# Optimization experiments

Hardware: AMD Instinct MI355X
Metric: run time of the kernel (lower is better)

The kernel has to match this reference:

```python
import jax, jax.numpy as jnp
import numpy as np

DIM = 1024
HEADS = 16
HEAD_DIM = DIM // HEADS


def setup_inputs() -> dict:
    key = jax.random.key(0)
    ks = jax.random.split(key, 9)
    s = 1.0 / np.sqrt(DIM)
    return {
        "x": jax.random.normal(ks[0], (2, 2048, DIM), dtype=jnp.float32),
        "Wq": jax.random.normal(ks[1], (DIM, DIM), dtype=jnp.float32) * s,
        "bq": jnp.zeros((DIM,), dtype=jnp.float32),
        "Wk": jax.random.normal(ks[2], (DIM, DIM), dtype=jnp.float32) * s,
        "bk": jnp.zeros((DIM,), dtype=jnp.float32),
        "Wv": jax.random.normal(ks[3], (DIM, DIM), dtype=jnp.float32) * s,
        "bv": jnp.zeros((DIM,), dtype=jnp.float32),
        "Wo": jax.random.normal(ks[4], (DIM, DIM), dtype=jnp.float32) * s,
        "bo": jnp.zeros((DIM,), dtype=jnp.float32),
    }


def reference(x, Wq, bq, Wk, bk, Wv, bv, Wo, bo):
    B, S, D = x.shape
    H, Dh = HEADS, HEAD_DIM

    def split_heads(t):  # (B,S,D) -> (B,H,S,Dh)
        return t.reshape(B, S, H, Dh).transpose(0, 2, 1, 3)

    q = split_heads(x @ Wq + bq)
    k = split_heads(x @ Wk + bk)
    v = split_heads(x @ Wv + bv)

    scores = jnp.einsum("bhsd,bhtd->bhst", q, k) / np.sqrt(Dh).astype(x.dtype)
    attn = jax.nn.softmax(scores, axis=-1)
    ctx = jnp.einsum("bhst,bhtd->bhsd", attn, v)
    ctx = ctx.transpose(0, 2, 1, 3).reshape(B, S, D)
    return ctx @ Wo + bo
```

## Files before the change

### kernel.cpp

```cpp
#include <hip/hip_runtime.h>
#include <hip/hip_bf16.h>
#include <cstdint>

typedef __bf16 bf16;
typedef __bf16 bf16x8 __attribute__((ext_vector_type(8)));
typedef float f32x4 __attribute__((ext_vector_type(4)));
typedef float f32x8 __attribute__((ext_vector_type(8)));
typedef float f32x16 __attribute__((ext_vector_type(16)));

#define DIM   1024
#define SEQ   2048
#define BATCH 2
#define HEADS 16
#define HDIM  64

#define QSCALE 0.1803368801111204f

__device__ __forceinline__ void gload_lds16(const void* g, void* l) {
    __builtin_amdgcn_global_load_lds(
        (const __attribute__((address_space(1))) void*)g,
        (__attribute__((address_space(3))) void*)l,
        16, 0, 0);
}

__device__ __forceinline__ uint32_t pkbf(float a, float b) {
    union { bf16 h[2]; uint32_t u; } t;
    t.h[0] = (bf16)a; t.h[1] = (bf16)b;
    return t.u;
}

#define LO8(v)  __builtin_shufflevector(v, v, 0, 1, 2, 3, 4, 5, 6, 7)
#define HI8(v)  __builtin_shufflevector(v, v, 8, 9, 10, 11, 12, 13, 14, 15)
#define LO4(v)  __builtin_shufflevector(v, v, 0, 1, 2, 3)
#define HI4(v)  __builtin_shufflevector(v, v, 4, 5, 6, 7)

__global__ __launch_bounds__(256) void cvt_wt_kernel(const float* __restrict__ Wq,
                                                     const float* __restrict__ Wk,
                                                     const float* __restrict__ Wv,
                                                     const float* __restrict__ Wo,
                                                     bf16* __restrict__ Wt) {
    int z = blockIdx.z;
    const float* W = (z == 0) ? Wq : (z == 1) ? Wk : (z == 2) ? Wv : Wo;
    bf16* out = Wt + (size_t)z * DIM * DIM;
    int w = threadIdx.x >> 6, lane = threadIdx.x & 63;
    int n  = blockIdx.x * 64 + lane;
    int kb = blockIdx.y * 32 + w * 8;
    bf16x8 o;
#pragma unroll
    for (int j = 0; j < 8; ++j)
        o[j] = (bf16)W[(size_t)(kb + j) * DIM + n];
    *(bf16x8*)(out + (size_t)n * DIM + kb) = o;
}

template <int MODE>
__global__ __launch_bounds__(256) void gemm128_kernel(
        const void* __restrict__ Ap,
        const bf16* __restrict__ WtB,
        const float* __restrict__ b0,
        const float* __restrict__ b1,
        const float* __restrict__ b2,
        void* __restrict__ outp) {
    constexpr int K  = DIM;
    constexpr int BN = (MODE == 1) ? 64 : 128;
    constexpr int NR = BN / 32;
    int z = (MODE == 0) ? blockIdx.z : 0;
    const bf16* Bt = WtB + (size_t)z * DIM * DIM;
    const float* bias = (MODE == 0) ? ((z == 0) ? b0 : (z == 1) ? b1 : b2) : b0;

    int m0 = blockIdx.y * 128, n0 = blockIdx.x * BN;
    int tid = threadIdx.x;
    int w = tid >> 6, lane = tid & 63, l15 = lane & 15, l4 = lane >> 4;
    int wr = (w >> 1) * 64, wc = (w & 1) * (BN / 2);

    __shared__ __align__(16) bf16 As[128 * 32];
    __shared__ __align__(16) bf16 Bs[BN * 32];

    int arow = tid >> 1, acol = (tid & 1) * 16;
    const float* asrc = (MODE == 0)
        ? (const float*)Ap + (size_t)(m0 + arow) * K + acol : nullptr;

    f32x4 acc[4][NR] = {};

    for (int k0 = 0; k0 < K; k0 += 32) {
#pragma unroll
        for (int rr = 0; rr < BN / 64; ++rr) {
            int c = rr * 256 + tid;
            gload_lds16(Bt + (size_t)(n0 + (c >> 2)) * K + k0 + (c & 3) * 8, &Bs[c * 8]);
        }
        if constexpr (MODE == 0) {
            const float4* s4 = (const float4*)(asrc + k0);
            float4 f0 = s4[0], f1 = s4[1], f2 = s4[2], f3 = s4[3];
            bf16x8 e0, e1;
            e0[0] = (bf16)f0.x; e0[1] = (bf16)f0.y; e0[2] = (bf16)f0.z; e0[3] = (bf16)f0.w;
            e0[4] = (bf16)f1.x; e0[5] = (bf16)f1.y; e0[6] = (bf16)f1.z; e0[7] = (bf16)f1.w;
            e1[0] = (bf16)f2.x; e1[1] = (bf16)f2.y; e1[2] = (bf16)f2.z; e1[3] = (bf16)f2.w;
            e1[4] = (bf16)f3.x; e1[5] = (bf16)f3.y; e1[6] = (bf16)f3.z; e1[7] = (bf16)f3.w;
            *(bf16x8*)&As[arow * 32 + acol]     = e0;
            *(bf16x8*)&As[arow * 32 + acol + 8] = e1;
        } else {
            const bf16* A = (const bf16*)Ap;
#pragma unroll
            for (int rr = 0; rr < 2; ++rr) {
                int c = rr * 256 + tid;
                gload_lds16(A + (size_t)(m0 + (c >> 2)) * K + k0 + (c & 3) * 8, &As[c * 8]);
            }
        }
        __syncthreads();
        bf16x8 af[4], bfr[NR];
#pragma unroll
        for (int m = 0; m < 4; ++m)
            af[m] = *(const bf16x8*)&As[(wr + m * 16 + l15) * 32 + l4 * 8];
#pragma unroll
        for (int n = 0; n < NR; ++n)
            bfr[n] = *(const bf16x8*)&Bs[(wc + n * 16 + l15) * 32 + l4 * 8];
#pragma unroll
        for (int m = 0; m < 4; ++m)
#pragma unroll
            for (int n = 0; n < NR; ++n)
                acc[m][n] = __builtin_amdgcn_mfma_f32_16x16x32_bf16(
                    af[m], bfr[n], acc[m][n], 0, 0, 0);
        __syncthreads();
    }

    float oscale = (MODE == 0 && z == 0) ? QSCALE : 1.0f;
#pragma unroll
    for (int n = 0; n < NR; ++n) {
        int col = n0 + wc + n * 16 + l15;
        float bv = bias[col];
#pragma unroll
        for (int m = 0; m < 4; ++m) {
            int rowb = m0 + wr + m * 16 + l4 * 4;
            if (MODE == 1) {
                float* out = (float*)outp;
#pragma unroll
                for (int i = 0; i < 4; ++i)
                    out[(size_t)(rowb + i) * DIM + col] = acc[m][n][i] + bv;
            } else if (z < 2) {
                bf16* out = (bf16*)outp + (size_t)z * (BATCH * HEADS * SEQ * HDIM);
                int h = col >> 6, d = col & 63;
#pragma unroll
                for (int i = 0; i < 4; ++i) {
                    int row = rowb + i;
                    int bb = row >> 11, s = row & 2047;
                    out[(((size_t)(bb * HEADS + h)) * SEQ + s) * HDIM + d] =
                        (bf16)((acc[m][n][i] + bv) * oscale);
                }
            } else {
                char* out = (char*)outp + (size_t)2 * (BATCH * HEADS * SEQ * HDIM) * 2;
                int h = col >> 6, d = col & 63;
                int dblk = d >> 5;
                int bb = rowb >> 11, s0 = rowb & 2047;
                int hb2 = bb * HEADS + h;
                int lane2 = (d & 31) + 32 * ((s0 >> 3) & 1);
                size_t off = (size_t)(hb2 * 64 + (s0 >> 5)) * 4096
                             + (dblk * 2 + ((s0 >> 4) & 1)) * 1024
                             + lane2 * 16 + (s0 & 7) * 2;
                union { bf16 hh[4]; ushort4 v; } pk;
#pragma unroll
                for (int i = 0; i < 4; ++i) pk.hh[i] = (bf16)(acc[m][n][i] + bv);
                *(ushort4*)(out + off) = pk.v;
            }
        }
    }
}

__global__ __launch_bounds__(256) void attn_kernel(const bf16* __restrict__ Q,
                                                   const bf16* __restrict__ K,
                                                   const bf16* __restrict__ Vf,
                                                   bf16* __restrict__ ctx) {
    int bid = blockIdx.x;
    int xcd = bid & 7, i = bid >> 3;
    int hb  = xcd * (BATCH * HEADS / 8) + (i >> 4);
    int q0  = (i & 15) * 128;
    int bb = hb >> 4, h = hb & 15;
    int tid = threadIdx.x, w = tid >> 6, lane = tid & 63;
    int l31 = lane & 31, hi = lane >> 5;

    const bf16* Qh = Q + (size_t)hb * SEQ * HDIM;
    const bf16* Kh = K + (size_t)hb * SEQ * HDIM;
    const char* Vh = (const char*)Vf + (size_t)hb * 64 * 4096 + lane * 16;

    __shared__ __align__(16) bf16 Ks[2][8192];

    int qrow = q0 + w * 32 + l31;
    bf16x8 qf[4];
#pragma unroll
    for (int ks = 0; ks < 4; ++ks)
        qf[ks] = *(const bf16x8*)&Qh[(size_t)qrow * HDIM + ks * 16 + hi * 8];

    f32x16 o0 = {}, o1 = {};
    float l = 0.f;

    const bf16* kbase[2];
    int ldsoff[2];
#pragma unroll
    for (int r = 0; r < 2; ++r) {
        int c = r * 256 + tid;
        int krow = c >> 3, kj = (c & 7) ^ (krow & 7);
        kbase[r] = Kh + (size_t)krow * HDIM + kj * 8;
        ldsoff[r] = c * 8;
    }
    auto stage = [&](bf16* ksd, int kv0) {
#pragma unroll
        for (int r = 0; r < 2; ++r) {
            gload_lds16(kbase[r] + (size_t)kv0 * HDIM,        ksd + ldsoff[r]);
            gload_lds16(kbase[r] + (size_t)(kv0 + 64) * HDIM, ksd + ldsoff[r] + 4096);
        }
    };

    int koffA = l31 * 128;
    int cb[4];
#pragma unroll
    for (int ks = 0; ks < 4; ++ks)
        cb[ks] = ((2 * ks + hi) ^ (l31 & 7)) << 4;

    auto sub64 = [&](const char* kp, const char* vjp) {
        f32x16 s0 = {}, s1 = {};
        __builtin_amdgcn_s_setprio(1);
#pragma unroll
        for (int ks = 0; ks < 4; ++ks) {
            bf16x8 k0 = *(const bf16x8*)(kp + koffA + cb[ks]);
            bf16x8 k1 = *(const bf16x8*)(kp + koffA + 4096 + cb[ks]);
            s0 = __builtin_amdgcn_mfma_f32_32x32x16_bf16(k0, qf[ks], s0, 0, 0, 0);
            s1 = __builtin_amdgcn_mfma_f32_32x32x16_bf16(k1, qf[ks], s1, 0, 0, 0);
        }
        __builtin_amdgcn_s_setprio(0);

        bf16x8 v0 = *(const bf16x8*)(vjp);
        bf16x8 v1 = *(const bf16x8*)(vjp + 1024);
        bf16x8 v2 = *(const bf16x8*)(vjp + 2048);
        bf16x8 v3 = *(const bf16x8*)(vjp + 3072);
        bf16x8 v4 = *(const bf16x8*)(vjp + 4096);
        bf16x8 v5 = *(const bf16x8*)(vjp + 5120);
        bf16x8 v6 = *(const bf16x8*)(vjp + 6144);
        bf16x8 v7 = *(const bf16x8*)(vjp + 7168);

#pragma unroll
        for (int r = 0; r < 16; ++r) {
            s0[r] = __builtin_amdgcn_exp2f(s0[r]);
            s1[r] = __builtin_amdgcn_exp2f(s1[r]);
        }

        f32x16 a16 = s0 + s1;
        f32x8  a8  = LO8(a16) + HI8(a16);
        f32x4  a4  = LO4(a8) + HI4(a8);
        l += (a4[0] + a4[1]) + (a4[2] + a4[3]);

        bf16x8 pa[4];
#pragma unroll
        for (int f2 = 0; f2 < 4; ++f2) {
            const f32x16& s = (f2 < 2) ? s0 : s1;
            int rb = (f2 & 1) * 8;
            uint32_t w0 = pkbf(s[rb + 0], s[rb + 1]), w1 = pkbf(s[rb + 2], s[rb + 3]);
            uint32_t w2 = pkbf(s[rb + 4], s[rb + 5]), w3 = pkbf(s[rb + 6], s[rb + 7]);
            asm("v_permlane32_swap_b32 %0, %1" : "+v"(w0), "+v"(w2));
            asm("v_permlane32_swap_b32 %0, %1" : "+v"(w1), "+v"(w3));
            union { uint32_t u[4]; bf16x8 v; } t2;
            t2.u[0] = w0; t2.u[1] = w1; t2.u[2] = w2; t2.u[3] = w3;
            pa[f2] = t2.v;
        }

        __builtin_amdgcn_s_setprio(1);
        o0 = __builtin_amdgcn_mfma_f32_32x32x16_bf16(v0, pa[0], o0, 0, 0, 0);
        o0 = __builtin_amdgcn_mfma_f32_32x32x16_bf16(v1, pa[1], o0, 0, 0, 0);
        o1 = __builtin_amdgcn_mfma_f32_32x32x16_bf16(v2, pa[0], o1, 0, 0, 0);
        o1 = __builtin_amdgcn_mfma_f32_32x32x16_bf16(v3, pa[1], o1, 0, 0, 0);
        o0 = __builtin_amdgcn_mfma_f32_32x32x16_bf16(v4, pa[2], o0, 0, 0, 0);
        o0 = __builtin_amdgcn_mfma_f32_32x32x16_bf16(v5, pa[3], o0, 0, 0, 0);
        o1 = __builtin_amdgcn_mfma_f32_32x32x16_bf16(v6, pa[2], o1, 0, 0, 0);
        o1 = __builtin_amdgcn_mfma_f32_32x32x16_bf16(v7, pa[3], o1, 0, 0, 0);
        __builtin_amdgcn_s_setprio(0);
    };

    auto proc = [&](const char* ksb, int kv0) {
        sub64(ksb,        Vh + (size_t)(kv0 >> 5) * 4096);
        sub64(ksb + 8192, Vh + (size_t)((kv0 + 64) >> 5) * 4096);
    };

    constexpr int NT = SEQ / 128;
    stage(Ks[0], 0);
    __syncthreads();

    for (int t = 0; t < NT; t += 2) {
        if (t + 1 < NT) stage(Ks[1], (t + 1) * 128);
        proc((const char*)&Ks[0][0], t * 128);
        __syncthreads();
        if (t + 2 < NT) stage(Ks[0], (t + 2) * 128);
        proc((const char*)&Ks[1][0], (t + 1) * 128);
        __syncthreads();
    }

    l += __shfl_xor(l, 32);
    float inv = 1.0f / l;
    size_t base = ((size_t)bb * SEQ + qrow) * DIM + h * HDIM;
#pragma unroll
    for (int g = 0; g < 4; ++g) {
        int dh0 = 8 * g + 4 * hi;
        union { bf16 hh[4]; ushort4 u; } a, b2;
#pragma unroll
        for (int i = 0; i < 4; ++i) {
            a.hh[i]  = (bf16)(o0[4 * g + i] * inv);
            b2.hh[i] = (bf16)(o1[4 * g + i] * inv);
        }
        *(ushort4*)&ctx[base + dh0]      = a.u;
        *(ushort4*)&ctx[base + 32 + dh0] = b2.u;
    }
}

extern "C" void kernel_launch(void* const* d_in, const int* in_sizes, int n_in,
                              void* d_out, int out_size, void* d_ws, size_t ws_size,
                              hipStream_t stream) {
    const float* x  = (const float*)d_in[0];
    const float* Wq = (const float*)d_in[1];
    const float* bq = (const float*)d_in[2];
    const float* Wk = (const float*)d_in[3];
    const float* bk = (const float*)d_in[4];
    const float* Wv = (const float*)d_in[5];
    const float* bv = (const float*)d_in[6];
    const float* Wo = (const float*)d_in[7];
    const float* bo = (const float*)d_in[8];

    char* ws = (char*)d_ws;
    bf16* Wt  = (bf16*)(ws + (8u  << 20));
    bf16* Qb  = (bf16*)(ws + (16u << 20));
    bf16* Kb  = (bf16*)(ws + (24u << 20));
    bf16* Vf  = (bf16*)(ws + (32u << 20));
    bf16* ctx = (bf16*)(ws + (40u << 20));

    cvt_wt_kernel<<<dim3(16, 32, 4), 256, 0, stream>>>(Wq, Wk, Wv, Wo, Wt);
    gemm128_kernel<0><<<dim3(8, 32, 3), 256, 0, stream>>>(x, Wt, bq, bk, bv, (void*)Qb);
    attn_kernel<<<512, 256, 0, stream>>>(Qb, Kb, Vf, ctx);
    gemm128_kernel<1><<<dim3(16, 32), 256, 0, stream>>>(
        ctx, Wt + (size_t)3 * DIM * DIM, bo, bo, bo, (void*)d_out);
}
```

Before: 121.3 us.

## Split attention KV range in two and merge partial outputs in a separate kernel

The attention kernel now splits each query tile's key/value sequence into two halves, doubling the grid to 1024 blocks. Each block writes an unnormalized bf16 partial context and its row sums, and a new merge kernel adds the two partials and divides by the combined sum. The aim is more blocks per CU, helped by a launch-bounds occupancy hint, so latency hides better. The cost is an extra kernel launch, extra global traffic for the partials, and bf16 rounding of unnormalized partials. The merge is only correct if both halves use the same softmax reference max, which cannot be checked from the visible code.

```diff
diff --git a/kernel.cpp b/kernel.cpp
--- a/kernel.cpp
+++ b/kernel.cpp
@@ -164,14 +164,19 @@
     }
 }
 
-__global__ __launch_bounds__(256) void attn_kernel(const bf16* __restrict__ Q,
-                                                   const bf16* __restrict__ K,
-                                                   const bf16* __restrict__ Vf,
-                                                   bf16* __restrict__ ctx) {
+__global__ __launch_bounds__(256, 4) void attn_kernel(const bf16* __restrict__ Q,
+                                                      const bf16* __restrict__ K,
+                                                      const bf16* __restrict__ Vf,
+                                                      bf16* __restrict__ op0,
+                                                      bf16* __restrict__ op1,
+                                                      float* __restrict__ lbuf) {
     int bid = blockIdx.x;
     int xcd = bid & 7, i = bid >> 3;
-    int hb  = xcd * (BATCH * HEADS / 8) + (i >> 4);
-    int q0  = (i & 15) * 128;
+    int hb  = xcd * 4 + (i >> 5);
+    int rem = i & 31;
+    int q0  = (rem >> 1) * 128;
+    int si  = rem & 1;
+    int kvb = si * (SEQ / 2);
     int bb = hb >> 4, h = hb & 15;
     int tid = threadIdx.x, w = tid >> 6, lane = tid & 63;
     int l31 = lane & 31, hi = lane >> 5;
@@ -277,21 +282,23 @@
         sub64(ksb + 8192, Vh + (size_t)((kv0 + 64) >> 5) * 4096);
     };
 
-    constexpr int NT = SEQ / 128;
-    stage(Ks[0], 0);
+    constexpr int NT = (SEQ / 2) / 128;
+    stage(Ks[0], kvb);
     __syncthreads();
 
     for (int t = 0; t < NT; t += 2) {
-        if (t + 1 < NT) stage(Ks[1], (t + 1) * 128);
-        proc((const char*)&Ks[0][0], t * 128);
+        if (t + 1 < NT) stage(Ks[1], kvb + (t + 1) * 128);
+        proc((const char*)&Ks[0][0], kvb + t * 128);
         __syncthreads();
-        if (t + 2 < NT) stage(Ks[0], (t + 2) * 128);
-        proc((const char*)&Ks[1][0], (t + 1) * 128);
+        if (t + 2 < NT) stage(Ks[0], kvb + (t + 2) * 128);
+        proc((const char*)&Ks[1][0], kvb + (t + 1) * 128);
         __syncthreads();
     }
 
     l += __shfl_xor(l, 32);
-    float inv = 1.0f / l;
+    bf16* op = si ? op1 : op0;
+    if (hi == 0)
+        lbuf[((size_t)si * BATCH * HEADS + hb) * SEQ + qrow] = l;
     size_t base = ((size_t)bb * SEQ + qrow) * DIM + h * HDIM;
 #pragma unroll
     for (int g = 0; g < 4; ++g) {
@@ -299,12 +306,35 @@
         union { bf16 hh[4]; ushort4 u; } a, b2;
 #pragma unroll
         for (int i = 0; i < 4; ++i) {
-            a.hh[i]  = (bf16)(o0[4 * g + i] * inv);
-            b2.hh[i] = (bf16)(o1[4 * g + i] * inv);
-        }
-        *(ushort4*)&ctx[base + dh0]      = a.u;
-        *(ushort4*)&ctx[base + 32 + dh0] = b2.u;
-    }
+            a.hh[i]  = (bf16)o0[4 * g + i];
+            b2.hh[i] = (bf16)o1[4 * g + i];
+        }
+        *(ushort4*)&op[base + dh0]      = a.u;
+        *(ushort4*)&op[base + 32 + dh0] = b2.u;
+    }
+}
+
+__global__ __launch_bounds__(256) void merge_kernel(const bf16* __restrict__ op0,
+                                                    const bf16* __restrict__ op1,
+                                                    const float* __restrict__ lbuf,
+                                                    bf16* __restrict__ ctx) {
+    int idx = blockIdx.x * 256 + threadIdx.x;
+    size_t e8 = (size_t)idx * 8;
+    int row = (int)(e8 >> 10);
+    int d   = (int)(e8 & 1023);
+    int h = d >> 6;
+    int bb = row >> 11, s = row & 2047;
+    int hb = bb * HEADS + h;
+    float la = lbuf[(size_t)hb * SEQ + s];
+    float lb = lbuf[((size_t)BATCH * HEADS + hb) * SEQ + s];
+    float inv = 1.0f / (la + lb);
+    bf16x8 a = *(const bf16x8*)&op0[e8];
+    bf16x8 b = *(const bf16x8*)&op1[e8];
+    bf16x8 o;
+#pragma unroll
+    for (int i = 0; i < 8; ++i)
+        o[i] = (bf16)(((float)a[i] + (float)b[i]) * inv);
+    *(bf16x8*)&ctx[e8] = o;
 }
 
 extern "C" void kernel_launch(void* const* d_in, const int* in_sizes, int n_in,
@@ -321,15 +351,18 @@
     const float* bo = (const float*)d_in[8];
 
     char* ws = (char*)d_ws;
-    bf16* Wt  = (bf16*)(ws + (8u  << 20));
-    bf16* Qb  = (bf16*)(ws + (16u << 20));
-    bf16* Kb  = (bf16*)(ws + (24u << 20));
-    bf16* Vf  = (bf16*)(ws + (32u << 20));
-    bf16* ctx = (bf16*)(ws + (40u << 20));
+    bf16*  op1  = (bf16*)ws;
+    bf16*  Wt   = (bf16*)(ws + (8u  << 20));
+    float* lbuf = (float*)(ws + (8u  << 20));
+    bf16*  Qb   = (bf16*)(ws + (16u << 20));
+    bf16*  Kb   = (bf16*)(ws + (24u << 20));
+    bf16*  Vf   = (bf16*)(ws + (32u << 20));
+    bf16*  op0  = (bf16*)(ws + (40u << 20));
 
     cvt_wt_kernel<<<dim3(16, 32, 4), 256, 0, stream>>>(Wq, Wk, Wv, Wo, Wt);
     gemm128_kernel<0><<<dim3(8, 32, 3), 256, 0, stream>>>(x, Wt, bq, bk, bv, (void*)Qb);
-    attn_kernel<<<512, 256, 0, stream>>>(Qb, Kb, Vf, ctx);
+    attn_kernel<<<1024, 256, 0, stream>>>(Qb, Kb, Vf, op0, op1, lbuf);
+    merge_kernel<<<2048, 256, 0, stream>>>(op0, op1, lbuf, op0);
     gemm128_kernel<1><<<dim3(16, 32), 256, 0, stream>>>(
-        ctx, Wt + (size_t)3 * DIM * DIM, bo, bo, bo, (void*)d_out);
-}
+        op0, Wt + (size_t)3 * DIM * DIM, bo, bo, bo, (void*)d_out);
+}
```

Result: slower. 189.9 us (+56.5%).
